# Optimization experiments

Measured on AMD Instinct MI355X. Metric: run time of the kernel, lower is better.

Reference implementation:

```python
import jax, jax.numpy as jnp
import numpy as np

E = 256; NH = 8; L = 1; P = 4; NQUEUE = 2
BEV_H = 200; BEV_W = 200; NQ = BEV_H * BEV_W; BS = 1; D = E // NH


def _conv2d(x, w):
    # 3x3, stride 1, padding 1, NCHW
    return jax.lax.conv_general_dilated(x, w, (1, 1), ((1, 1), (1, 1)),
                                         dimension_numbers=('NCHW', 'OIHW', 'NCHW'))


def setup_inputs() -> dict:
    key = jax.random.key(0)
    ks = jax.random.split(key, 16)
    inp = {
        'query': jax.random.normal(ks[0], (NQ, BS, E), jnp.float32),
        'key': jax.random.normal(ks[1], (NQ, BS, E), jnp.float32),
        'value': jax.random.normal(ks[2], (NQ, BS, E), jnp.float32),
        'query_pos': jax.random.normal(ks[3], (NQ, BS, E), jnp.float32),
        'reference_points': jax.random.uniform(ks[4], (BS, NQ, 1, 2), jnp.float32),
        'spatial_shapes': jnp.array([[BEV_H, BEV_W]], jnp.int32),
        'level_start_index': jnp.array([0], jnp.int32),
        'pre_bev_feat': jax.random.normal(ks[5], (NQ, BS, E), jnp.float32),
        'pre_ref_points': jax.random.uniform(ks[6], (BS, NQ, 1, 2), jnp.float32),
        'start_of_sequence': jnp.zeros((BS,), bool),
        'Wv': jax.random.normal(ks[7], (E, E), jnp.float32) * (1.0 / np.sqrt(E)),
        'bv': jnp.zeros((E,), jnp.float32),
        'Wo': jax.random.normal(ks[8], (E, E), jnp.float32) * (1.0 / np.sqrt(E)),
        'bo': jnp.zeros((E,), jnp.float32),
        'off_w': jax.random.normal(ks[9], (NQUEUE * NH * L * P * 2, 2 * E, 3, 3), jnp.float32) * 0.02,
        'off_b': jnp.zeros((NQUEUE * NH * L * P * 2,), jnp.float32),
        'attn_w': jax.random.normal(ks[10], (NQUEUE * NH * L * P, 2 * E, 3, 3), jnp.float32) * 0.02,
        'attn_b': jnp.zeros((NQUEUE * NH * L * P,), jnp.float32),
    }
    return inp


def reference(query, key, value, query_pos, reference_points, spatial_shapes,
              level_start_index, pre_bev_feat, pre_ref_points, start_of_sequence,
              Wv, bv, Wo, bo, off_w, off_b, attn_w, attn_b):
    bs = query.shape[1]
    # reset previous BEV feat at sequence starts
    pre = jnp.where(start_of_sequence[None, :, None], query, pre_bev_feat)
    val = jnp.concatenate([pre, query], axis=1)          # (NQ, 2bs, E)
    identity = query
    q = query + query_pos
    q = q.transpose(1, 0, 2)                              # (bs, NQ, E)
    val = val.transpose(1, 0, 2)                          # (2bs, NQ, E)
    # qv_cat: concat prev-frame value with query
    q = jnp.concatenate([val[:bs], q], axis=-1)           # (bs, NQ, 2E)
    valp = (val @ Wv.T + bv).reshape(2 * bs, NQ, NH, D)   # (2bs, HW, NH, D)

    qbev = q.transpose(0, 2, 1).reshape(bs, 2 * E, BEV_H, BEV_W)
    off = _conv2d(qbev, off_w) + off_b[None, :, None, None]
    off = off.reshape(bs, -1, NQ).transpose(0, 2, 1)
    off = off.reshape(bs, NQ, NH, NQUEUE, L, P, 2)
    aw = _conv2d(qbev, attn_w) + attn_b[None, :, None, None]
    aw = aw.reshape(bs, -1, NQ).transpose(0, 2, 1)
    aw = aw.reshape(bs, NQ, NH, NQUEUE, L * P)
    aw = jax.nn.softmax(aw, axis=-1).reshape(bs, NQ, NH, NQUEUE, L, P)
    aw = aw.transpose(3, 0, 1, 2, 4, 5).reshape(2 * bs, NQ, NH, L, P)
    off = off.transpose(3, 0, 1, 2, 4, 5, 6).reshape(2 * bs, NQ, NH, L, P, 2)

    ref2d = jnp.concatenate([pre_ref_points, reference_points[:, :, 0:1, :2]], axis=0)  # (2bs,NQ,1,2)
    norm = jnp.stack([spatial_shapes[:, 1], spatial_shapes[:, 0]], -1).astype(off.dtype)  # (L,2) (w,h)
    loc = ref2d[:, :, None, :, None, :] + off / norm[None, None, None, :, None, :]  # (2bs,NQ,NH,L,P,2)

    # --- multiscale deformable attention core (single level, bilinear, zero pad, align_corners=False) ---
    loc0 = loc[:, :, :, 0]                                # (2bs,NQ,NH,P,2)
    x = loc0[..., 0] * BEV_W - 0.5
    y = loc0[..., 1] * BEV_H - 0.5
    x0 = jnp.floor(x); y0 = jnp.floor(y)
    fx = x - x0; fy = y - y0
    x0i = x0.astype(jnp.int32); y0i = y0.astype(jnp.int32)
    val_t = valp.transpose(0, 2, 1, 3)                    # (2bs, NH, HW, D)

    def corner(xi, yi, w):
        valid = (xi >= 0) & (xi < BEV_W) & (yi >= 0) & (yi < BEV_H)
        idx = jnp.clip(yi, 0, BEV_H - 1) * BEV_W + jnp.clip(xi, 0, BEV_W - 1)  # (2bs,NQ,NH,P)
        idx_t = idx.transpose(0, 2, 1, 3).reshape(2 * bs, NH, NQ * P)
        g = jnp.take_along_axis(val_t, idx_t[..., None], axis=2)               # (2bs,NH,NQ*P,D)
        g = g.reshape(2 * bs, NH, NQ, P, D)
        wv = (w * valid).transpose(0, 2, 1, 3)             # (2bs,NH,NQ,P)
        return g * wv[..., None]

    samp = (corner(x0i, y0i, (1 - fx) * (1 - fy))
            + corner(x0i + 1, y0i, fx * (1 - fy))
            + corner(x0i, y0i + 1, (1 - fx) * fy)
            + corner(x0i + 1, y0i + 1, fx * fy))          # (2bs,NH,NQ,P,D)

    out = jnp.einsum('bhqpd,bqhp->bqhd', samp, aw[:, :, :, 0])  # (2bs,NQ,NH,D)
    out = out.reshape(2 * bs, NQ, E)
    out = (out[:bs] + out[bs:]) / NQUEUE                  # average the two bev queues
    out = out @ Wo.T + bo                                 # (bs,NQ,E)
    out = out.transpose(1, 0, 2)                          # (NQ,bs,E)
    return out + identity
```

## Files before the change

### kernel.cpp

```cpp
#include <hip/hip_runtime.h>
#include <math.h>

#define NQ    40000
#define EDIM  256
#define BEVH  200
#define BEVW  200

enum { A_IM2COL = 0, A_VAL = 1, A_PLAIN = 2 };
enum { OUT_F32 = 0, OUT_VSLAB = 1, OUT_CONV = 2, OUT_F32ADD = 3 };

typedef __attribute__((ext_vector_type(8))) short bf16x8;
typedef __attribute__((ext_vector_type(4))) short bf16x4;
typedef __attribute__((ext_vector_type(4))) float f32x4;

typedef __attribute__((address_space(3))) unsigned int lds_u32_t;
typedef const __attribute__((address_space(1))) unsigned int g_u32_t;
#define GLOAD_LDS16(g, l) __builtin_amdgcn_global_load_lds((g_u32_t*)(g), (lds_u32_t*)(l), 16, 0, 0)

__device__ __forceinline__ short f2bf(float f) {
  union { float f; unsigned u; } uu; uu.f = f;
  unsigned r = (uu.u + 0x7fff + ((uu.u >> 16) & 1)) >> 16;
  return (short)r;
}
__device__ __forceinline__ float bf2f(short s) {
  union { unsigned u; float f; } v;
  v.u = ((unsigned)(unsigned short)s) << 16;
  return v.f;
}

__global__ __launch_bounds__(256) void pad_kernel(
    const float* __restrict__ query, const float* __restrict__ qpos,
    const float* __restrict__ prebev, const unsigned char* __restrict__ sos,
    short* __restrict__ img, short* __restrict__ qbf)
{
  const int TOT = 203 * 202 * 64;
  int t = blockIdx.x * 256 + threadIdx.x;
  if (t >= TOT) return;
  int s = t * 8;
  int pr = s / (202 * 512);
  int rem = s - pr * (202 * 512);
  int px = rem >> 9;
  int c = rem & 511;
  int y = pr - 1, x = px - 1;

  bf16x8 o;
#pragma unroll
  for (int j = 0; j < 8; j++) o[j] = 0;

  if (y >= 0 && y < BEVH && x >= 0 && x < BEVW) {
    int n = y * BEVW + x;
    if (c < 256) {
      bool sf = sos[0] != 0;
      const float* p = (sf ? query : prebev) + (size_t)n * 256 + c;
      float4 v0 = *(const float4*)p;
      float4 v1 = *(const float4*)(p + 4);
      o[0] = f2bf(v0.x); o[1] = f2bf(v0.y); o[2] = f2bf(v0.z); o[3] = f2bf(v0.w);
      o[4] = f2bf(v1.x); o[5] = f2bf(v1.y); o[6] = f2bf(v1.z); o[7] = f2bf(v1.w);
    } else {
      const float* pq = query + (size_t)n * 256 + (c - 256);
      const float* pp = qpos + (size_t)n * 256 + (c - 256);
      float4 q0 = *(const float4*)pq, q1 = *(const float4*)(pq + 4);
      float4 p0 = *(const float4*)pp, p1 = *(const float4*)(pp + 4);
      bf16x8 qo;
      qo[0] = f2bf(q0.x); qo[1] = f2bf(q0.y); qo[2] = f2bf(q0.z); qo[3] = f2bf(q0.w);
      qo[4] = f2bf(q1.x); qo[5] = f2bf(q1.y); qo[6] = f2bf(q1.z); qo[7] = f2bf(q1.w);
      *(bf16x8*)&qbf[(size_t)n * 256 + (c - 256)] = qo;
      o[0] = f2bf(q0.x + p0.x); o[1] = f2bf(q0.y + p0.y);
      o[2] = f2bf(q0.z + p0.z); o[3] = f2bf(q0.w + p0.w);
      o[4] = f2bf(q1.x + p1.x); o[5] = f2bf(q1.y + p1.y);
      o[6] = f2bf(q1.z + p1.z); o[7] = f2bf(q1.w + p1.w);
    }
  }
  *(bf16x8*)&img[s] = o;
}

__global__ __launch_bounds__(256) void reorder_cat_kernel(
    const float* __restrict__ off_w, const float* __restrict__ off_b,
    const float* __restrict__ attn_w, const float* __restrict__ attn_b,
    short* __restrict__ wcat, float* __restrict__ bcat)
{
  int i = blockIdx.x * 256 + threadIdx.x;
  if (i < 192) bcat[i] = i < 128 ? off_b[i] : attn_b[i - 128];
  if (i >= 192 * 4608) return;
  int co = i / 4608;
  int r = i - co * 4608;
  int tap = r >> 9, ci = r & 511;
  float v = co < 128 ? off_w[(size_t)co * 4608 + ci * 9 + tap]
                     : attn_w[(size_t)(co - 128) * 4608 + ci * 9 + tap];
  wcat[i] = f2bf(v);
}

__global__ __launch_bounds__(256) void wcast_kernel(
    const float* __restrict__ Wv, const float* __restrict__ Wo,
    short* __restrict__ wvb, short* __restrict__ wob)
{
  int t = blockIdx.x * 256 + threadIdx.x;
  if (t >= 16384) return;
  const float* src = t < 8192 ? Wv + (size_t)t * 8 : Wo + (size_t)(t - 8192) * 8;
  short* dst = t < 8192 ? wvb + (size_t)t * 8 : wob + (size_t)(t - 8192) * 8;
  float4 v0 = *(const float4*)src, v1 = *(const float4*)(src + 4);
  bf16x8 o;
  o[0] = f2bf(v0.x); o[1] = f2bf(v0.y); o[2] = f2bf(v0.z); o[3] = f2bf(v0.w);
  o[4] = f2bf(v1.x); o[5] = f2bf(v1.y); o[6] = f2bf(v1.z); o[7] = f2bf(v1.w);
  *(bf16x8*)dst = o;
}

template <int AMODE, int KTOT, int TBM, int TBN, int OUTMODE>
__global__ __launch_bounds__(256) void mfma_gemm_kernel(
    const short* __restrict__ A0, const short* __restrict__ A1,
    const short* __restrict__ Bw, const float* __restrict__ bias,
    const float* __restrict__ addend,
    float* __restrict__ Cf, short* __restrict__ Cb, int M)
{
  constexpr int A_ISS = TBM / 32;
  constexpr int B_ISS = TBN / 32;
  constexpr int MR = TBM / 32;
  constexpr int NR = TBN / 32;

  __shared__ __align__(16) short As[TBM * 64];
  __shared__ __align__(16) short Bs[TBN * 64];

  const int tid = threadIdx.x;
  const int wv = tid >> 6, lane = tid & 63;
  const int wr_ = wv >> 1, wc = wv & 1;

  int bx = blockIdx.x;
  if constexpr (AMODE == A_IM2COL) {
    int xcd = bx & 7, pos = bx >> 3;
    bx = (xcd < 1 ? xcd * 79 : 79 + (xcd - 1) * 78) + pos;
  }
  const int m0 = bx * TBM;
  const int n0 = blockIdx.y * TBN;

  const int csw = ((lane & 7) ^ ((lane >> 3) & 7)) * 8;

  const short* ap[A_ISS];
#pragma unroll
  for (int i = 0; i < A_ISS; i++) {
    int m = m0 + (i * 4 + wv) * 8 + (lane >> 3);
    if constexpr (AMODE == A_IM2COL) {
      int y = m / BEVW;
      int x = m - y * BEVW;
      ap[i] = A0 + ((size_t)y * 202 + x) * 512 + csw;
    } else if constexpr (AMODE == A_VAL) {
      if (m < NQ) {
        int y = m / BEVW;
        int x = m - y * BEVW;
        ap[i] = A0 + ((size_t)(y + 1) * 202 + (x + 1)) * 512 + csw;
      } else {
        ap[i] = A1 + (size_t)(m - NQ) * 256 + csw;
      }
    } else {
      int mc = m < M ? m : M - 1;
      ap[i] = A0 + (size_t)mc * KTOT + csw;
    }
  }
  const short* bp[B_ISS];
#pragma unroll
  for (int i = 0; i < B_ISS; i++) {
    int r = n0 + (i * 4 + wv) * 8 + (lane >> 3);
    bp[i] = Bw + (size_t)r * KTOT + csw;
  }

  f32x4 acc[MR][NR];
#pragma unroll
  for (int mr = 0; mr < MR; mr++)
#pragma unroll
    for (int nr = 0; nr < NR; nr++) acc[mr][nr] = (f32x4){0.f, 0.f, 0.f, 0.f};

  for (int k0 = 0; k0 < KTOT; k0 += 64) {
    int koff;
    if constexpr (AMODE == A_IM2COL) {
      int tap = k0 >> 9, c0 = k0 & 511;
      int ty = tap / 3, txp = tap - ty * 3;
      koff = (ty * 202 + txp) * 512 + c0;
    } else {
      koff = k0;
    }

#pragma unroll
    for (int i = 0; i < A_ISS; i++)
      GLOAD_LDS16(ap[i] + koff, &As[(i * 4 + wv) * 512]);
#pragma unroll
    for (int i = 0; i < B_ISS; i++)
      GLOAD_LDS16(bp[i] + k0, &Bs[(i * 4 + wv) * 512]);

    __syncthreads();

#pragma unroll
    for (int ks = 0; ks < 2; ks++) {
      const int kk = ks * 32 + (lane >> 4) * 8;
      bf16x8 af[MR], bfr[NR];
#pragma unroll
      for (int mr = 0; mr < MR; mr++) {
        int row = wr_ * (TBM / 2) + mr * 16 + (lane & 15);
        af[mr] = *(const bf16x8*)&As[row * 64 + (kk ^ ((row & 7) << 3))];
      }
#pragma unroll
      for (int nr = 0; nr < NR; nr++) {
        int row = wc * (TBN / 2) + nr * 16 + (lane & 15);
        bfr[nr] = *(const bf16x8*)&Bs[row * 64 + (kk ^ ((row & 7) << 3))];
      }
#pragma unroll
      for (int mr = 0; mr < MR; mr++)
#pragma unroll
        for (int nr = 0; nr < NR; nr++)
          acc[mr][nr] = __builtin_amdgcn_mfma_f32_16x16x32_bf16(
              af[mr], bfr[nr], acc[mr][nr], 0, 0, 0);
    }
    __syncthreads();
  }

#pragma unroll
  for (int mr = 0; mr < MR; mr++) {
#pragma unroll
    for (int nr = 0; nr < NR; nr++) {
      int col = n0 + wc * (TBN / 2) + nr * 16 + (lane & 15);
      float bsv = bias[col];
#pragma unroll
      for (int r = 0; r < 4; r++) {
        int grow = m0 + wr_ * (TBM / 2) + mr * 16 + (lane >> 4) * 4 + r;
        if (grow < M) {
          float o = acc[mr][nr][r] + bsv;
          if constexpr (OUTMODE == OUT_VSLAB) {
            int b = grow >= NQ;
            int n = grow - (b ? NQ : 0);
            int hh = col >> 5, d = col & 31;
            Cb[((size_t)(hh * 2 + b) * NQ + n) * 32 + d] = f2bf(o);
          } else if constexpr (OUTMODE == OUT_CONV) {
            int hh, j;
            if (col < 128) { hh = col >> 4; j = col & 15; }
            else { int c = col - 128; hh = c >> 3; j = 16 + (c & 7); }
            Cf[((size_t)hh * NQ + grow) * 24 + j] = o;
          } else if constexpr (OUTMODE == OUT_F32ADD) {
            o += addend[(size_t)grow * 256 + col];
            Cf[(size_t)grow * 256 + col] = o;
          } else {
            Cf[(size_t)grow * 256 + col] = o;
          }
        }
      }
    }
  }
}

__global__ __launch_bounds__(256) void sample_kernel(
    const short* __restrict__ valpb, const float* __restrict__ convall,
    const float* __restrict__ preref, const float* __restrict__ refp,
    short* __restrict__ midb)
{
  int id = blockIdx.x;
  int h = id & 7, q = id >> 3;
  int wv = threadIdx.x >> 6, lane = threadIdx.x & 63;
  int n = q * 32 + wv * 8 + (lane >> 3);
  int g = lane & 7;

  const float* cv = convall + ((size_t)h * NQ + n) * 24;
  f32x4 acc = (f32x4){0.f, 0.f, 0.f, 0.f};

#pragma unroll
  for (int b = 0; b < 2; b++) {
    const float* rp = b ? refp : preref;
    float rx = rp[(size_t)n * 2 + 0] * 200.f - 0.5f;
    float ry = rp[(size_t)n * 2 + 1] * 200.f - 0.5f;

    float4 o01 = *(const float4*)(cv + b * 8);
    float4 o23 = *(const float4*)(cv + b * 8 + 4);
    float ox[4] = {o01.x, o01.z, o23.x, o23.z};
    float oy[4] = {o01.y, o01.w, o23.y, o23.w};

    float4 a = *(const float4*)(cv + 16 + b * 4);
    float mx = fmaxf(fmaxf(a.x, a.y), fmaxf(a.z, a.w));
    float e0 = __expf(a.x - mx), e1 = __expf(a.y - mx);
    float e2 = __expf(a.z - mx), e3 = __expf(a.w - mx);
    float inv = 1.f / (e0 + e1 + e2 + e3);
    float aw[4] = {e0 * inv, e1 * inv, e2 * inv, e3 * inv};

    const short* vb = valpb + ((size_t)(h * 2 + b) * NQ) * 32 + g * 4;

#pragma unroll
    for (int p = 0; p < 4; p++) {
      float x = rx + ox[p];
      float y = ry + oy[p];
      float x0f = floorf(x), y0f = floorf(y);
      float fx = x - x0f, fy = y - y0f;
      int x0 = (int)x0f, y0 = (int)y0f;
      float wt[4] = {(1.f - fx) * (1.f - fy), fx * (1.f - fy),
                     (1.f - fx) * fy, fx * fy};
      int xs[4] = {x0, x0 + 1, x0, x0 + 1};
      int ys[4] = {y0, y0, y0 + 1, y0 + 1};
#pragma unroll
      for (int c = 0; c < 4; c++) {
        if (xs[c] >= 0 && xs[c] < BEVW && ys[c] >= 0 && ys[c] < BEVH) {
          bf16x4 v = *(const bf16x4*)&vb[(size_t)(ys[c] * BEVW + xs[c]) * 32];
          float cw = aw[p] * wt[c];
          acc[0] += cw * bf2f(v[0]);
          acc[1] += cw * bf2f(v[1]);
          acc[2] += cw * bf2f(v[2]);
          acc[3] += cw * bf2f(v[3]);
        }
      }
    }
  }

  bf16x4 m4;
#pragma unroll
  for (int j = 0; j < 4; j++) m4[j] = f2bf(acc[j] * 0.5f);
  *(bf16x4*)&midb[(size_t)n * 256 + h * 32 + g * 4] = m4;
}

extern "C" void kernel_launch(void* const* d_in, const int* in_sizes, int n_in,
                              void* d_out, int out_size, void* d_ws, size_t ws_size,
                              hipStream_t stream)
{
  const float* query  = (const float*)d_in[0];
  const float* qpos   = (const float*)d_in[3];
  const float* refp   = (const float*)d_in[4];
  const float* prebev = (const float*)d_in[7];
  const float* preref = (const float*)d_in[8];
  const unsigned char* sos = (const unsigned char*)d_in[9];
  const float* Wv     = (const float*)d_in[10];
  const float* bv     = (const float*)d_in[11];
  const float* Wo     = (const float*)d_in[12];
  const float* bo     = (const float*)d_in[13];
  const float* off_w  = (const float*)d_in[14];
  const float* off_b  = (const float*)d_in[15];
  const float* attn_w = (const float*)d_in[16];
  const float* attn_b = (const float*)d_in[17];
  float* out = (float*)d_out;

  float* convall = (float*)d_ws;
  short* valpb  = (short*)(convall + 7680000);
  short* img    = valpb + 20480000;
  short* qbf    = img + 20996672;
  short* midb   = qbf + 10240000;
  short* wcat   = midb + 10240000;
  short* wvb    = wcat + 884736;
  short* wob    = wvb + 65536;
  float* bcat   = (float*)(wob + 65536);

  pad_kernel<<<dim3((203 * 202 * 64 + 255) / 256), dim3(256), 0, stream>>>(
      query, qpos, prebev, sos, img, qbf);
  reorder_cat_kernel<<<dim3((192 * 4608 + 255) / 256), dim3(256), 0, stream>>>(
      off_w, off_b, attn_w, attn_b, wcat, bcat);
  wcast_kernel<<<dim3(64), dim3(256), 0, stream>>>(Wv, Wo, wvb, wob);

  mfma_gemm_kernel<A_VAL, 256, 128, 64, OUT_VSLAB>
      <<<dim3(625, 4), dim3(256), 0, stream>>>(
      img, qbf, wvb, bv, nullptr, nullptr, valpb, 2 * NQ);

  mfma_gemm_kernel<A_IM2COL, 4608, 64, 192, OUT_CONV>
      <<<dim3(625, 1), dim3(256), 0, stream>>>(
      img, nullptr, wcat, bcat, nullptr, convall, nullptr, NQ);

  sample_kernel<<<dim3(10000), dim3(256), 0, stream>>>(
      valpb, convall, preref, refp, midb);

  mfma_gemm_kernel<A_PLAIN, 256, 128, 64, OUT_F32ADD>
      <<<dim3(313, 4), dim3(256), 0, stream>>>(
      midb, nullptr, wob, bo, query, out, nullptr, NQ);

  (void)in_sizes; (void)n_in; (void)out_size; (void)ws_size;
}
```

Measured before the change: 460.7 us.

## Double-buffer LDS tiles in MFMA GEMM to overlap global loads with compute

Splits the GEMM's shared-memory A/B tiles into two buffers and issues the next K-tile's global-to-LDS loads before computing on the current one. Explicit vmcnt waits and raw s_barrier calls replace the __syncthreads pair, so the MFMA work can hide the load latency. This doubles LDS use per block, which may lower occupancy. The waitcnt values are hard-coded per issue count, so any new tile configuration needs a matching case added.

New measurement: 524.1 us. 1.14x slower.

```diff
diff --git a/kernel.cpp b/kernel.cpp
--- a/kernel.cpp
+++ b/kernel.cpp
@@ -16,6 +16,13 @@
 typedef __attribute__((address_space(3))) unsigned int lds_u32_t;
 typedef const __attribute__((address_space(1))) unsigned int g_u32_t;
 #define GLOAD_LDS16(g, l) __builtin_amdgcn_global_load_lds((g_u32_t*)(g), (lds_u32_t*)(l), 16, 0, 0)
+
+template <int N> __device__ __forceinline__ void vmwait() {
+  if constexpr (N == 0) asm volatile("s_waitcnt vmcnt(0)" ::: "memory");
+  else if constexpr (N == 6) asm volatile("s_waitcnt vmcnt(6)" ::: "memory");
+  else if constexpr (N == 8) asm volatile("s_waitcnt vmcnt(8)" ::: "memory");
+  else static_assert(N == 0 || N == 6 || N == 8, "add vmcnt case");
+}
 
 __device__ __forceinline__ short f2bf(float f) {
   union { float f; unsigned u; } uu; uu.f = f;
@@ -114,11 +121,13 @@
 {
   constexpr int A_ISS = TBM / 32;
   constexpr int B_ISS = TBN / 32;
+  constexpr int ISS = A_ISS + B_ISS;
   constexpr int MR = TBM / 32;
   constexpr int NR = TBN / 32;
-
-  __shared__ __align__(16) short As[TBM * 64];
-  __shared__ __align__(16) short Bs[TBN * 64];
+  constexpr int NT = KTOT / 64;
+
+  __shared__ __align__(16) short As[2][TBM * 64];
+  __shared__ __align__(16) short Bs[2][TBN * 64];
 
   const int tid = threadIdx.x;
   const int wv = tid >> 6, lane = tid & 63;
@@ -162,31 +171,51 @@
     bp[i] = Bw + (size_t)r * KTOT + csw;
   }
 
-  f32x4 acc[MR][NR];
-#pragma unroll
-  for (int mr = 0; mr < MR; mr++)
-#pragma unroll
-    for (int nr = 0; nr < NR; nr++) acc[mr][nr] = (f32x4){0.f, 0.f, 0.f, 0.f};
-
-  for (int k0 = 0; k0 < KTOT; k0 += 64) {
-    int koff;
+  auto koff_of = [&](int t) -> int {
     if constexpr (AMODE == A_IM2COL) {
+      int k0 = t * 64;
       int tap = k0 >> 9, c0 = k0 & 511;
       int ty = tap / 3, txp = tap - ty * 3;
-      koff = (ty * 202 + txp) * 512 + c0;
+      return (ty * 202 + txp) * 512 + c0;
     } else {
-      koff = k0;
-    }
-
+      return t * 64;
+    }
+  };
+
+  auto stage = [&](int buf, int t) {
+    int koff = koff_of(t);
+    short* Ab = &As[buf][0];
+    short* Bb = &Bs[buf][0];
 #pragma unroll
     for (int i = 0; i < A_ISS; i++)
-      GLOAD_LDS16(ap[i] + koff, &As[(i * 4 + wv) * 512]);
+      GLOAD_LDS16(ap[i] + koff, Ab + (i * 4 + wv) * 512);
+    int k0 = t * 64;
 #pragma unroll
     for (int i = 0; i < B_ISS; i++)
-      GLOAD_LDS16(bp[i] + k0, &Bs[(i * 4 + wv) * 512]);
-
-    __syncthreads();
-
+      GLOAD_LDS16(bp[i] + k0, Bb + (i * 4 + wv) * 512);
+  };
+
+  f32x4 acc[MR][NR];
+#pragma unroll
+  for (int mr = 0; mr < MR; mr++)
+#pragma unroll
+    for (int nr = 0; nr < NR; nr++) acc[mr][nr] = (f32x4){0.f, 0.f, 0.f, 0.f};
+
+  stage(0, 0);
+
+  for (int t = 0; t < NT; ++t) {
+    const int cur = t & 1;
+    if (t + 1 < NT) {
+      stage(cur ^ 1, t + 1);
+      vmwait<ISS>();
+    } else {
+      vmwait<0>();
+    }
+    __builtin_amdgcn_s_barrier();
+    __builtin_amdgcn_sched_barrier(0);
+
+    const short* Ab = &As[cur][0];
+    const short* Bb = &Bs[cur][0];
 #pragma unroll
     for (int ks = 0; ks < 2; ks++) {
       const int kk = ks * 32 + (lane >> 4) * 8;
@@ -194,12 +223,12 @@
 #pragma unroll
       for (int mr = 0; mr < MR; mr++) {
         int row = wr_ * (TBM / 2) + mr * 16 + (lane & 15);
-        af[mr] = *(const bf16x8*)&As[row * 64 + (kk ^ ((row & 7) << 3))];
+        af[mr] = *(const bf16x8*)&Ab[row * 64 + (kk ^ ((row & 7) << 3))];
       }
 #pragma unroll
       for (int nr = 0; nr < NR; nr++) {
         int row = wc * (TBN / 2) + nr * 16 + (lane & 15);
-        bfr[nr] = *(const bf16x8*)&Bs[row * 64 + (kk ^ ((row & 7) << 3))];
+        bfr[nr] = *(const bf16x8*)&Bb[row * 64 + (kk ^ ((row & 7) << 3))];
       }
 #pragma unroll
       for (int mr = 0; mr < MR; mr++)
@@ -208,7 +237,8 @@
           acc[mr][nr] = __builtin_amdgcn_mfma_f32_16x16x32_bf16(
               af[mr], bfr[nr], acc[mr][nr], 0, 0, 0);
     }
-    __syncthreads();
+    __builtin_amdgcn_sched_barrier(0);
+    __builtin_amdgcn_s_barrier();
   }
 
 #pragma unroll
```
